# Kernel optimization log

Hardware: AMD Instinct MI355X
Metric: run time of the kernel (lower is better)

The kernel has to match this reference:

```python
import jax, jax.numpy as jnp
import numpy as np
import math
from jax import lax

PI = math.pi


def setup_inputs() -> dict:
    key = jax.random.key(0)
    k1, k2, k3, k4, k5 = jax.random.split(key, 5)
    B, L, F, FSIZE, FS = 128, 2048, 64, 129, 16000
    input_tensor = jax.random.normal(k1, (B, L, 2), dtype=jnp.float32)
    # normalized mel center frequencies b1/fs in [-0.5, 0.5]
    fc = jax.random.uniform(k2, (F,), dtype=jnp.float32, minval=-0.5, maxval=0.5)
    # normalized bandwidths (b2-b1)/(2 fs), small positive
    fbandwidth = jax.random.uniform(k3, (F,), dtype=jnp.float32, minval=0.001, maxval=0.05)
    time_length = jax.random.uniform(k4, (F,), dtype=jnp.float32, minval=L / 10.0, maxval=float(L))
    start_time = jax.random.uniform(k5, (F,), dtype=jnp.float32, minval=0.0, maxval=float(L) / 2.0)
    return {
        "input_tensor": input_tensor,
        "fc": fc,
        "fbandwidth": fbandwidth,
        "time_length": time_length,
        "start_time": start_time,
        "fsize": FSIZE,
        "fs": FS,
    }


def reference(input_tensor, fc, fbandwidth, time_length, start_time, fsize, fs):
    B, L, _ = input_tensor.shape
    F = fc.shape[0]
    K = (fsize - 1) // 2
    fs_f = float(fs)

    # constant grids (match tf build())
    t_right = jnp.linspace(1.0, (fsize - 1) / 2.0, K, dtype=jnp.float32) / fs_f  # (K,)
    n = jnp.linspace(0.0, float(fsize), fsize, dtype=jnp.float32)                 # (fsize,)
    window = 0.54 - 0.46 * jnp.cos(2.0 * PI * n / float(fsize))                   # (fsize,)

    # --- per-filter Gaussian time masks ---
    t = jnp.arange(L, dtype=jnp.float32)
    center = (start_time + time_length) / 2.0                                     # (F,)
    std = time_length / 1.665                                                     # (F,)
    gauss = jnp.exp(-0.5 * jnp.square((t[None, :] - center[:, None]) / (std[:, None] + 1e-9)))  # (F,L)
    gauss = gauss / (jnp.max(gauss, axis=1, keepdims=True) + 1e-9)
    mask = jnp.transpose(gauss)[None, :, :]                                       # (1,L,F)

    real_m = input_tensor[:, :, 0:1] * mask                                       # (B,L,F)
    imag_m = input_tensor[:, :, 1:2] * mask                                       # (B,L,F)

    # --- dynamic sinc bandpass filters ---
    band = fbandwidth * fs_f                                                      # (F,)
    arg = 2.0 * PI * band[:, None] * t_right[None, :]                              # (F,K)
    y_right = jnp.sin(arg) / arg
    bp = jnp.concatenate([y_right[:, ::-1], jnp.ones((F, 1), jnp.float32), y_right], axis=1)  # (F,fsize)
    bp = bp * (2.0 * band[:, None])
    bp = bp * window
    bp = bp / (jnp.max(jnp.abs(bp), axis=1, keepdims=True) + 1e-9)

    phase = 2.0 * PI * fc[:, None] * n[None, :]                                    # (F,fsize)
    kr = jnp.transpose(bp * jnp.cos(phase))[:, None, :]                            # (fsize,1,F)
    ki = jnp.transpose(bp * jnp.sin(phase))[:, None, :]                            # (fsize,1,F)

    def dconv(x, k):  # depthwise 1D conv, SAME padding (cross-correlation, matches TF)
        return lax.conv_general_dilated(
            x, k, window_strides=(1,), padding="SAME",
            dimension_numbers=("NWC", "WIO", "NWC"), feature_group_count=F)

    out_rr = dconv(real_m, kr)
    out_ii = dconv(imag_m, ki)
    out_ri = dconv(real_m, ki)
    out_ir = dconv(imag_m, kr)

    out_real = out_rr - out_ii
    out_imag = out_ri + out_ir
    return jnp.concatenate([out_real, out_imag], axis=2)                           # (B,L,2F)
```

## Files before the change

### kernel.cpp

```cpp
#include <hip/hip_runtime.h>
#include <math.h>


#define PI_F 3.14159265358979323846f
#define L_LEN 2048
#define F_N   64
#define FSIZE 129
#define FS_F  16000.0f

__global__ void prep_filters(const float* __restrict__ fc,
                             const float* __restrict__ fbw,
                             float2* __restrict__ krki)
{
    const int f   = blockIdx.x;
    const int tid = threadIdx.x;
    __shared__ float red[256];

    const float band = fbw[f] * FS_F;
    float bp = 0.0f;
    if (tid < FSIZE) {
        float y;
        const int m = tid - 64;
        if (m == 0) {
            y = 1.0f;
        } else {
            const float tr  = (float)abs(m) / FS_F;
            const float arg = 2.0f * PI_F * band * tr;
            y = __sinf(arg) / arg;
        }
        const float nn  = (float)tid * (129.0f / 128.0f);
        const float win = 0.54f - 0.46f * __cosf(2.0f * PI_F * nn / 129.0f);
        bp = y * (2.0f * band) * win;
    }
    red[tid] = fabsf(bp);
    __syncthreads();
    for (int s = 128; s > 0; s >>= 1) {
        if (tid < s) red[tid] = fmaxf(red[tid], red[tid + s]);
        __syncthreads();
    }
    const float inv = 1.0f / (red[0] + 1e-9f);
    if (tid < FSIZE) {
        const float v  = bp * inv;
        const float ph = 2.0f * PI_F * fc[f] * ((float)tid * (129.0f / 128.0f));
        float sn, cs;
        __sincosf(ph, &sn, &cs);
        krki[tid * F_N + f] = make_float2(v * cs, v * sn);
    }
}

__global__ __launch_bounds__(256, 3)
void sinc_conv(const float* __restrict__ in,
               const float2* __restrict__ krki,
               const float* __restrict__ tl,
               const float* __restrict__ st,
               float* __restrict__ out)
{
    const int tid = threadIdx.x;
    const int wv  = tid >> 6;
    const int f   = tid & 63;
    const int nlb = L_LEN / 64;
    const int b   = blockIdx.x / nlb;
    const int lw  = (blockIdx.x % nlb) * 64 + wv * 16;

    const float tlv  = tl[f];
    const float stv  = st[f];
    const float c_f  = (stv + tlv) * 0.5f;
    const float sd   = tlv * (1.0f / 1.665f) + 1e-9f;
    const float rsd  = 1.0f / sd;
    const float tn   = floorf(c_f + 0.5f);
    const float zm   = (tn - c_f) * rsd;
    const float minv = 1.0f / (__expf(-0.5f * zm * zm) + 1e-9f);

    const float* inb = in + (size_t)b * (L_LEN * 2);

    auto loadY = [&](int p) -> float2 {
        const int   pc = min(max(p, 0), L_LEN - 1);
        const float2 v = *reinterpret_cast<const float2*>(inb + pc * 2);
        const float zz = ((float)p - c_f) * rsd;
        const float m  = __expf(-0.5f * zz * zz) * minv;
        const bool ok  = (p >= 0) && (p < L_LEN);
        return make_float2(ok ? v.x * m : 0.0f, ok ? v.y * m : 0.0f);
    };

    float2 w[16];
    float  ar[16], ai[16];
#pragma unroll
    for (int j = 0; j < 16; ++j) { ar[j] = 0.0f; ai[j] = 0.0f; }
#pragma unroll
    for (int j = 0; j < 16; ++j) w[j] = loadY(lw - 64 + j);
    float2 ynext = loadY(lw - 48);

    const float2* kp = krki + f;
    float2 kv = kp[0];

#pragma unroll 1
    for (int k0 = 0; k0 < 8; ++k0) {
#pragma unroll
        for (int kk = 0; kk < 16; ++kk) {
            const int k = (k0 << 4) + kk;
            const float2 kvn = kp[(size_t)(k + 1) * F_N];
#pragma unroll
            for (int j = 0; j < 16; ++j) {
                const int s = (kk + j) & 15;
                ar[j] = fmaf(w[s].x,  kv.x, ar[j]);
                ar[j] = fmaf(w[s].y, -kv.y, ar[j]);
                ai[j] = fmaf(w[s].x,  kv.y, ai[j]);
                ai[j] = fmaf(w[s].y,  kv.x, ai[j]);
            }
            w[kk] = ynext;
            ynext = loadY(lw + k - 47);
            kv = kvn;
        }
    }
    {
#pragma unroll
        for (int j = 0; j < 16; ++j) {
            ar[j] = fmaf(w[j].x,  kv.x, ar[j]);
            ar[j] = fmaf(w[j].y, -kv.y, ar[j]);
            ai[j] = fmaf(w[j].x,  kv.y, ai[j]);
            ai[j] = fmaf(w[j].y,  kv.x, ai[j]);
        }
    }

    float* ob = out + ((size_t)b * L_LEN + lw) * (2 * F_N);
#pragma unroll
    for (int j = 0; j < 16; ++j) {
        ob[j * (2 * F_N) + f]       = ar[j];
        ob[j * (2 * F_N) + F_N + f] = ai[j];
    }
}

extern "C" void kernel_launch(void* const* d_in, const int* in_sizes, int n_in,
                              void* d_out, int out_size, void* d_ws, size_t ws_size,
                              hipStream_t stream)
{
    const float* in  = (const float*)d_in[0];
    const float* fc  = (const float*)d_in[1];
    const float* fbw = (const float*)d_in[2];
    const float* tl  = (const float*)d_in[3];
    const float* st  = (const float*)d_in[4];

    const int B = in_sizes[0] / (L_LEN * 2);

    float2* krki = (float2*)d_ws;

    prep_filters<<<F_N, 256, 0, stream>>>(fc, fbw, krki);
    sinc_conv<<<B * (L_LEN / 64), 256, 0, stream>>>(in, krki, tl, st, (float*)d_out);
}
```

Before: 389.7 us.

## Pre-pad input and compute Gaussian mask by recurrence instead of per-sample exp

Adds a pre-pass kernel that copies the input into a zero-padded buffer, so the convolution inner loop needs no clamping or bounds predicates. The per-sample Gaussian mask exp is replaced by a multiplicative recurrence (m *= u; u *= d), leaving only a few exps per thread. Launch bounds are raised to 4 blocks per SM. This trades an extra kernel launch and an extra pass over the input in global memory, plus accumulated float rounding in the recurrence, for fewer transcendental and branch instructions in the hot loop.

```diff
diff --git a/kernel.cpp b/kernel.cpp
--- a/kernel.cpp
+++ b/kernel.cpp
@@ -7,6 +7,9 @@
 #define F_N   64
 #define FSIZE 129
 #define FS_F  16000.0f
+#define PADL  64
+#define PADR  80
+#define PROW  (PADL + L_LEN + PADR)
 
 __global__ void prep_filters(const float* __restrict__ fc,
                              const float* __restrict__ fbw,
@@ -48,8 +51,20 @@
     }
 }
 
-__global__ __launch_bounds__(256, 3)
-void sinc_conv(const float* __restrict__ in,
+__global__ void prep_pad(const float* __restrict__ in, float2* __restrict__ pad, int B)
+{
+    const int idx = blockIdx.x * 256 + threadIdx.x;
+    if (idx >= B * PROW) return;
+    const int b = idx / PROW;
+    const int i = idx - b * PROW;
+    const int p = i - PADL;
+    float2 v = make_float2(0.0f, 0.0f);
+    if (p >= 0 && p < L_LEN) v = reinterpret_cast<const float2*>(in)[b * L_LEN + p];
+    pad[idx] = v;
+}
+
+__global__ __launch_bounds__(256, 4)
+void sinc_conv(const float2* __restrict__ pad,
                const float2* __restrict__ krki,
                const float* __restrict__ tl,
                const float* __restrict__ st,
@@ -62,64 +77,63 @@
     const int b   = blockIdx.x / nlb;
     const int lw  = (blockIdx.x % nlb) * 64 + wv * 16;
 
-    const float tlv  = tl[f];
-    const float stv  = st[f];
-    const float c_f  = (stv + tlv) * 0.5f;
-    const float sd   = tlv * (1.0f / 1.665f) + 1e-9f;
-    const float rsd  = 1.0f / sd;
-    const float tn   = floorf(c_f + 0.5f);
-    const float zm   = (tn - c_f) * rsd;
-    const float minv = 1.0f / (__expf(-0.5f * zm * zm) + 1e-9f);
+    const float tlv = tl[f];
+    const float stv = st[f];
+    const float c_f = (stv + tlv) * 0.5f;
+    const float sd  = tlv * (1.0f / 1.665f) + 1e-9f;
+    const float rs  = 1.0f / sd;
+    const float i2  = 0.5f * rs * rs;
+    const float zn  = (floorf(c_f + 0.5f) - c_f) * rs;
+    const float minv = 1.0f / (__expf(-0.5f * zn * zn) + 1e-9f);
 
-    const float* inb = in + (size_t)b * (L_LEN * 2);
+    const float p0 = (float)(lw - 64);
+    float m = __expf(-(p0 - c_f) * (p0 - c_f) * i2) * minv;
+    float u = __expf((2.0f * (c_f - p0) - 1.0f) * i2);
+    const float d = __expf(-2.0f * i2);
 
-    auto loadY = [&](int p) -> float2 {
-        const int   pc = min(max(p, 0), L_LEN - 1);
-        const float2 v = *reinterpret_cast<const float2*>(inb + pc * 2);
-        const float zz = ((float)p - c_f) * rsd;
-        const float m  = __expf(-0.5f * zz * zz) * minv;
-        const bool ok  = (p >= 0) && (p < L_LEN);
-        return make_float2(ok ? v.x * m : 0.0f, ok ? v.y * m : 0.0f);
-    };
+    const float2* xb = pad + (size_t)b * PROW + (PADL + lw - 64);
+    const float2* tb = krki + f;
 
     float2 w[16];
     float  ar[16], ai[16];
 #pragma unroll
-    for (int j = 0; j < 16; ++j) { ar[j] = 0.0f; ai[j] = 0.0f; }
-#pragma unroll
-    for (int j = 0; j < 16; ++j) w[j] = loadY(lw - 64 + j);
-    float2 ynext = loadY(lw - 48);
+    for (int j = 0; j < 16; ++j) {
+        const float2 xv = xb[j];
+        w[j] = make_float2(xv.x * m, xv.y * m);
+        m *= u; u *= d;
+        ar[j] = 0.0f; ai[j] = 0.0f;
+    }
 
-    const float2* kp = krki + f;
-    float2 kv = kp[0];
+    const float2* xs = xb + 16;
+    float2 tv = tb[0];
 
 #pragma unroll 1
     for (int k0 = 0; k0 < 8; ++k0) {
+        const float2* xk = xs + (k0 << 4);
+        const float2* tk = tb + (size_t)((k0 << 4) + 1) * F_N;
 #pragma unroll
         for (int kk = 0; kk < 16; ++kk) {
-            const int k = (k0 << 4) + kk;
-            const float2 kvn = kp[(size_t)(k + 1) * F_N];
+            const float2 tnx = tk[(size_t)kk * F_N];
+            const float2 xnx = xk[kk];
 #pragma unroll
             for (int j = 0; j < 16; ++j) {
                 const int s = (kk + j) & 15;
-                ar[j] = fmaf(w[s].x,  kv.x, ar[j]);
-                ar[j] = fmaf(w[s].y, -kv.y, ar[j]);
-                ai[j] = fmaf(w[s].x,  kv.y, ai[j]);
-                ai[j] = fmaf(w[s].y,  kv.x, ai[j]);
+                ar[j] = fmaf(w[s].x,  tv.x, ar[j]);
+                ar[j] = fmaf(w[s].y, -tv.y, ar[j]);
+                ai[j] = fmaf(w[s].x,  tv.y, ai[j]);
+                ai[j] = fmaf(w[s].y,  tv.x, ai[j]);
             }
-            w[kk] = ynext;
-            ynext = loadY(lw + k - 47);
-            kv = kvn;
+            w[kk] = make_float2(xnx.x * m, xnx.y * m);
+            m *= u; u *= d;
+            tv = tnx;
         }
     }
-    {
 #pragma unroll
-        for (int j = 0; j < 16; ++j) {
-            ar[j] = fmaf(w[j].x,  kv.x, ar[j]);
-            ar[j] = fmaf(w[j].y, -kv.y, ar[j]);
-            ai[j] = fmaf(w[j].x,  kv.y, ai[j]);
-            ai[j] = fmaf(w[j].y,  kv.x, ai[j]);
-        }
+    for (int j = 0; j < 16; ++j) {
+        ar[j] = fmaf(w[j].x,  tv.x, ar[j]);
+        ar[j] = fmaf(w[j].y, -tv.y, ar[j]);
+        ai[j] = fmaf(w[j].x,  tv.y, ai[j]);
+        ai[j] = fmaf(w[j].y,  tv.x, ai[j]);
     }
 
     float* ob = out + ((size_t)b * L_LEN + lw) * (2 * F_N);
@@ -143,7 +157,9 @@
     const int B = in_sizes[0] / (L_LEN * 2);
 
     float2* krki = (float2*)d_ws;
+    float2* pad  = (float2*)((char*)d_ws + 66048);
 
     prep_filters<<<F_N, 256, 0, stream>>>(fc, fbw, krki);
-    sinc_conv<<<B * (L_LEN / 64), 256, 0, stream>>>(in, krki, tl, st, (float*)d_out);
+    prep_pad<<<(B * PROW + 255) / 256, 256, 0, stream>>>(in, pad, B);
+    sinc_conv<<<B * (L_LEN / 64), 256, 0, stream>>>(pad, krki, tl, st, (float*)d_out);
 }
```

Measured after the change: 567.8 us. 45.7% more time.
